# Kernel tuning notes

Hardware: AMD Instinct MI355X
Metric: run time of the kernel (lower is better)

The kernel has to match this reference:

```python
import jax, jax.numpy as jnp
import numpy as np
from jax import lax

B, C, H, L = 4, 64, 8, 2048  # batch, per-head channels, heads, sequence length


def setup_inputs() -> dict:
    key = jax.random.key(0)
    ks = jax.random.split(key, 15)

    def p(k, shape, s=0.05):
        return jax.random.normal(k, shape, jnp.float32) * s

    inp = {"x": jax.random.normal(ks[0], (B, C, L), jnp.float32)}
    for i, nm in enumerate(["q", "k", "v"]):
        inp[f"{nm}_dw"] = p(ks[1 + 4 * i], (C, 1, 3))       # depthwise conv weight, groups=C, k=3
        inp[f"{nm}_db"] = p(ks[2 + 4 * i], (C,))
        inp[f"{nm}_pw"] = p(ks[3 + 4 * i], (H * C, C))      # pointwise 1x1 conv weight
        inp[f"{nm}_pb"] = p(ks[4 + 4 * i], (H * C,))
    inp["u_w"] = p(ks[13], (C, H * C))                      # unify_heads 1x1 conv weight
    inp["u_b"] = p(ks[14], (C,))
    return inp


def dsconv(x, dw, db, pw, pb):
    # Depth-separable conv1d: depthwise (k=3, pad=1, groups=C) then pointwise 1x1.
    c = x.shape[1]
    y = lax.conv_general_dilated(x, dw, window_strides=(1,), padding=[(1, 1)],
                                 dimension_numbers=("NCH", "OIH", "NCH"),
                                 feature_group_count=c)
    y = y + db[None, :, None]
    return jnp.einsum("bcl,oc->bol", y, pw) + pb[None, :, None]


def reference(x, q_dw, q_db, q_pw, q_pb, k_dw, k_db, k_pw, k_pb,
              v_dw, v_db, v_pw, v_pb, u_w, u_b):
    b, c, l = x.shape
    h = H
    scale = c ** (-0.25)
    q = dsconv(x, q_dw, q_db, q_pw, q_pb).reshape(b, h, c, l) * scale
    k = dsconv(x, k_dw, k_db, k_pw, k_pb).reshape(b, h, c, l) * scale
    v = dsconv(x, v_dw, v_db, v_pw, v_pb).reshape(b, h, c, l)
    # dot[b,h,i,j] = sum_c k[b,h,c,i] * q[b,h,c,j]  (i = key pos, j = query pos)
    dot = jnp.einsum("bhci,bhcj->bhij", k, q)
    att = jax.nn.softmax(dot, axis=2)  # normalize over key positions (torch dim=1 of [bh,l,l])
    out = jnp.einsum("bhci,bhij->bhcj", v, att).reshape(b, h * c, l)
    return jnp.einsum("bkl,ck->bcl", out, u_w) + u_b[None, :, None]
```

## Files before the change

### kernel.cpp

```cpp
#include <hip/hip_runtime.h>
#include <hip/hip_bf16.h>
#include <stdint.h>
#include <string.h>

typedef unsigned short u16;
typedef unsigned int u32;
typedef __bf16 bf16x8 __attribute__((ext_vector_type(8)));
typedef float f32x4 __attribute__((ext_vector_type(4)));
typedef unsigned int u32x2v __attribute__((ext_vector_type(2)));

#define NB 4
#define NC 64
#define NH 8
#define NL 2048
#define HC 512

#define XT_OFF  ((size_t)0)
#define WM_OFF  ((size_t)1 << 20)
#define PBM_OFF ((size_t)2 << 20)
#define V_OFF   ((size_t)4 << 20)
#define QT_OFF  ((size_t)12 << 20)
#define KT_OFF  ((size_t)20 << 20)

#define LP 68

#if __has_builtin(__builtin_amdgcn_exp2f)
#define EXP2F __builtin_amdgcn_exp2f
#else
#define EXP2F exp2f
#endif

static __device__ __forceinline__ u16 f2bfu(float f) {
  union { float f; unsigned int i; } x; x.f = f;
  unsigned int i = x.i;
  return (u16)((i + 0x7fffu + ((i >> 16) & 1u)) >> 16);
}
static __device__ __forceinline__ u32 pk2(float a, float b) {
  float2 f; f.x = a; f.y = b;
  __hip_bfloat162 h = __float22bfloat162_rn(f);
  u32 w; __builtin_memcpy(&w, &h, 4); return w;
}
static __device__ __forceinline__ bf16x8 ld_bf8(const u16* p) {
  bf16x8 v; __builtin_memcpy(&v, p, 16); return v;
}
static __device__ __forceinline__ bf16x8 frag_from4(u32 a, u32 b, u32 c, u32 d) {
  u32 t[4] = {a, b, c, d};
  bf16x8 v; __builtin_memcpy(&v, t, 16); return v;
}

#define XCHG(X_, Y_, Fa_, Fb_)                                              \
  {                                                                         \
    u32x2v a_ = __builtin_amdgcn_permlane32_swap((X_), (Y_), false, false); \
    u32x2v b_ = __builtin_amdgcn_permlane16_swap(a_.x, a_.y, false, false); \
    Fa_ = b_.x; Fb_ = b_.y;                                                 \
  }

__global__ __launch_bounds__(256) void prep_all(
    const float* __restrict__ x,
    const float* __restrict__ qdw, const float* __restrict__ qdb,
    const float* __restrict__ qpw, const float* __restrict__ qpb,
    const float* __restrict__ kdw, const float* __restrict__ kdb,
    const float* __restrict__ kpw, const float* __restrict__ kpb,
    const float* __restrict__ vdw, const float* __restrict__ vdb,
    const float* __restrict__ vpw, const float* __restrict__ vpb,
    const float* __restrict__ ub,
    u16* __restrict__ Wm, float* __restrict__ pbm,
    u16* __restrict__ xT, float* __restrict__ out)
{
  __shared__ __align__(16) u16 T[64 * LP];
  int bx = blockIdx.x;
  int tid = threadIdx.x;

  if (bx < 512) {
    int i4 = bx * 256 + tid;
    int c = (i4 >> 9) & 63;
    float f = ub[c];
    float4 v = {f, f, f, f};
    ((float4*)out)[i4] = v;
    return;
  }
  if (bx < 902) {
    int idx = (bx - 512) * 256 + tid;
    if (idx < 98304) {
      int tns = idx >> 15, r = idx & 32767, o = r >> 6, c = r & 63;
      const float* dw = (tns == 0) ? qdw : (tns == 1) ? kdw : vdw;
      const float* pw = (tns == 0) ? qpw : (tns == 1) ? kpw : vpw;
      float s = (tns == 0) ? 0.35355339059327373f * 1.4426950408889634f
              : (tns == 1) ? 0.35355339059327373f : 1.0f;
      float w = pw[o * 64 + c] * s;
#pragma unroll
      for (int d = 0; d < 3; ++d)
        Wm[((size_t)(tns * 3 + d) * 512 + o) * 64 + c] = f2bfu(w * dw[c * 3 + d]);
    } else {
      int i = idx - 98304;
      int tns = i >> 9, o = i & 511;
      const float* db = (tns == 0) ? qdb : (tns == 1) ? kdb : vdb;
      const float* pw = (tns == 0) ? qpw : (tns == 1) ? kpw : vpw;
      const float* pb = (tns == 0) ? qpb : (tns == 1) ? kpb : vpb;
      float s = (tns == 0) ? 0.35355339059327373f * 1.4426950408889634f
              : (tns == 1) ? 0.35355339059327373f : 1.0f;
      float bias = pb[o];
      for (int c = 0; c < 64; ++c) bias += pw[o * 64 + c] * db[c];
      pbm[i] = bias * s;
    }
    return;
  }
  {
    int b2 = bx - 902;
    int lt = b2 & 31, b = b2 >> 5;
    {
      int c = tid & 63, ls = (tid >> 6) * 16;
      const float4* g = (const float4*)(x + ((size_t)b * NC + c) * NL + lt * 64 + ls);
      u16 tmp[16];
#pragma unroll
      for (int j4 = 0; j4 < 4; ++j4) {
        float4 f = g[j4];
        tmp[j4*4+0] = f2bfu(f.x); tmp[j4*4+1] = f2bfu(f.y);
        tmp[j4*4+2] = f2bfu(f.z); tmp[j4*4+3] = f2bfu(f.w);
      }
#pragma unroll
      for (int j = 0; j < 16; ++j) T[(ls + j) * LP + c] = tmp[j];
    }
    __syncthreads();
    {
      int r = tid >> 2, cs = (tid & 3) * 16;
      uint4 a = *(const uint4*)&T[r * LP + cs];
      uint4 b3 = *(const uint4*)&T[r * LP + cs + 8];
      u16* o = xT + ((size_t)b * NL + lt * 64 + r) * 64 + cs;
      *(uint4*)o = a;
      *(uint4*)(o + 8) = b3;
    }
  }
}

__global__ __launch_bounds__(256) void qkv_gemm(
    const u16* __restrict__ xT, const u16* __restrict__ Wm,
    const float* __restrict__ pbm,
    u16* __restrict__ v, u16* __restrict__ qT, u16* __restrict__ kT)
{
  __shared__ __align__(16) u16 WS[3][64 * LP];
  __shared__ __align__(16) u16 XS[2][66 * LP];
  __shared__ __align__(16) u16 OS[64 * LP];

  int bx = blockIdx.x;
  int lg  = bx & 7;
  int och = (bx >> 3) & 7;
  int tmp = bx >> 6;
  int tns = tmp % 3;
  int b   = tmp / 3;

  int tid = threadIdx.x;
  int wave = tid >> 6, lane = tid & 63, quad = lane >> 4, l16 = lane & 15;
  const u16* xg = xT + (size_t)b * NL * 64;

  {
    const u16* wg = Wm + ((size_t)(tns * 3) * 512 + och * 64) * 64;
#pragma unroll
    for (int it = 0; it < 6; ++it) {
      int s = tid + it * 256;
      int d = s >> 9, r = s & 511;
      int o = r >> 3, c4 = r & 7;
      uint4 w = *(const uint4*)(wg + ((size_t)d * 512 + o) * 64 + c4 * 8);
      *(uint4*)&WS[d][o * LP + c4 * 8] = w;
    }
  }

  int xr0 = tid >> 3,          xc0 = (tid & 7) * 8;
  int xr1 = (tid + 256) >> 3,  xc1 = xc0;
  int xr2 = (tid + 512) >> 3,  xc2 = xc0;
  uint4 R0, R1, R2;
  uint4 Z = {0, 0, 0, 0};

#define LOAD_XS(tt)                                                         \
  {                                                                         \
    int base = (lg * 4 + (tt)) * 64 - 1;                                    \
    int g0 = base + xr0, g1 = base + xr1, g2 = base + xr2;                  \
    R0 = ((unsigned)g0 < NL) ? *(const uint4*)(xg + (size_t)g0 * 64 + xc0) : Z; \
    R1 = ((unsigned)g1 < NL) ? *(const uint4*)(xg + (size_t)g1 * 64 + xc1) : Z; \
    if (tid < 16)                                                           \
      R2 = ((unsigned)g2 < NL) ? *(const uint4*)(xg + (size_t)g2 * 64 + xc2) : Z; \
  }
#define STORE_XS(bf)                                                        \
  {                                                                         \
    *(uint4*)&XS[bf][xr0 * LP + xc0] = R0;                                  \
    *(uint4*)&XS[bf][xr1 * LP + xc1] = R1;                                  \
    if (tid < 16) *(uint4*)&XS[bf][xr2 * LP + xc2] = R2;                    \
  }

  LOAD_XS(0); STORE_XS(0);
  LOAD_XS(1);
  __syncthreads();

  float bias4[4];
  bf16x8 aw[3][2];
  if (tns == 2) {
    const float* pbt = pbm + tns * 512 + och * 64 + wave * 16;
#pragma unroll
    for (int rr = 0; rr < 4; ++rr) bias4[rr] = pbt[quad * 4 + rr];
#pragma unroll
    for (int d = 0; d < 3; ++d)
#pragma unroll
      for (int kh = 0; kh < 2; ++kh)
        aw[d][kh] = ld_bf8(&WS[d][(wave * 16 + l16) * LP + kh * 32 + quad * 8]);
  } else {
    const float* pbt = pbm + tns * 512 + och * 64;
#pragma unroll
    for (int nt = 0; nt < 4; ++nt) bias4[nt] = pbt[nt * 16 + l16];
  }

  for (int t = 0; t < 4; ++t) {
    int cur = t & 1;
    f32x4 acc[4] = {{0,0,0,0},{0,0,0,0},{0,0,0,0},{0,0,0,0}};

    if (tns == 2) {
#pragma unroll
      for (int nt = 0; nt < 4; ++nt)
#pragma unroll
        for (int d = 0; d < 3; ++d)
#pragma unroll
          for (int kh = 0; kh < 2; ++kh) {
            bf16x8 bx8 = ld_bf8(&XS[cur][(nt * 16 + l16 + d) * LP + kh * 32 + quad * 8]);
            acc[nt] = __builtin_amdgcn_mfma_f32_16x16x32_bf16(aw[d][kh], bx8, acc[nt], 0, 0, 0);
          }
    } else {
      bf16x8 ax[3][2];
#pragma unroll
      for (int d = 0; d < 3; ++d)
#pragma unroll
        for (int kh = 0; kh < 2; ++kh)
          ax[d][kh] = ld_bf8(&XS[cur][(wave * 16 + l16 + d) * LP + kh * 32 + quad * 8]);
#pragma unroll
      for (int nt = 0; nt < 4; ++nt)
#pragma unroll
        for (int d = 0; d < 3; ++d)
#pragma unroll
          for (int kh = 0; kh < 2; ++kh) {
            bf16x8 bw = ld_bf8(&WS[d][(nt * 16 + l16) * LP + kh * 32 + quad * 8]);
            acc[nt] = __builtin_amdgcn_mfma_f32_16x16x32_bf16(ax[d][kh], bw, acc[nt], 0, 0, 0);
          }
    }

    if (t < 3) { STORE_XS((t + 1) & 1); if (t < 2) LOAD_XS(t + 2); }
    __syncthreads();

    if (tns == 2) {
#pragma unroll
      for (int nt = 0; nt < 4; ++nt)
#pragma unroll
        for (int rr = 0; rr < 4; ++rr)
          OS[(wave * 16 + quad * 4 + rr) * LP + nt * 16 + l16] =
              f2bfu(acc[nt][rr] + bias4[rr]);
    } else {
#pragma unroll
      for (int nt = 0; nt < 4; ++nt)
#pragma unroll
        for (int rr = 0; rr < 4; ++rr)
          OS[(wave * 16 + quad * 4 + rr) * LP + nt * 16 + l16] =
              f2bfu(acc[nt][rr] + bias4[nt]);
    }
    __syncthreads();

    {
      int lt = lg * 4 + t;
      int r = tid >> 2, ck = (tid & 3) * 16;
      uint4 a = *(const uint4*)&OS[r * LP + ck];
      uint4 b2 = *(const uint4*)&OS[r * LP + ck + 8];
      u16* gp;
      if (tns == 2)
        gp = v + ((size_t)(b * HC + och * 64 + r)) * NL + lt * 64 + ck;
      else {
        u16* dst = (tns == 0) ? qT : kT;
        gp = dst + ((size_t)(b * 8 + och) * NL + lt * 64 + r) * 64 + ck;
      }
      *(uint4*)gp = a;
      *(uint4*)(gp + 8) = b2;
    }
  }
#undef LOAD_XS
#undef STORE_XS
}

__global__ __launch_bounds__(256) void attn_kernel(
    const u16* __restrict__ qT, const u16* __restrict__ kT,
    const u16* __restrict__ vg, const float* __restrict__ uw,
    float* __restrict__ outg)
{
  __shared__ __align__(16) u16 Kt[2][64 * LP];
  __shared__ __align__(16) u16 Vt[2][64 * LP];
  __shared__ __align__(16) u16 UW[64 * LP];

  int bx = blockIdx.x;
  int qt = bx & 15, bh = bx >> 4;
  int b = bh >> 3, h = bh & 7;
  int tid = threadIdx.x;
  int wave = tid >> 6, lane = tid & 63, quad = lane >> 4, l16 = lane & 15;

  const u16* Qh = qT + (size_t)bh * NL * 64;
  const u16* Kh = kT + (size_t)bh * NL * 64;
  const u16* Vh = vg + ((size_t)(b * HC + h * NC)) * NL;
  int q0 = qt * 128;

  int sr = tid >> 2, ss = (tid & 3) * 16;
  int vc = tid & 63, vk = (tid >> 6) * 16;

  {
    int c = tid >> 2, g = (tid & 3) * 16;
    const float4* s = (const float4*)(uw + (size_t)c * HC + h * 64 + g);
#pragma unroll
    for (int j = 0; j < 4; ++j) {
      float4 w = s[j];
      u16* d = &UW[c * LP + g + j * 4];
      d[0] = f2bfu(w.x); d[1] = f2bfu(w.y); d[2] = f2bfu(w.z); d[3] = f2bfu(w.w);
    }
  }

  uint4 ka, kb, va, vb;
  {
    const u16* ks = Kh + (size_t)sr * 64 + ss;
    ka = *(const uint4*)ks; kb = *(const uint4*)(ks + 8);
    const u16* vs = Vh + (size_t)vc * NL + vk;
    va = *(const uint4*)vs; vb = *(const uint4*)(vs + 8);
    *(uint4*)&Kt[0][sr * LP + ss] = ka;
    *(uint4*)&Kt[0][sr * LP + ss + 8] = kb;
    *(uint4*)&Vt[0][vc * LP + vk] = va;
    *(uint4*)&Vt[0][vc * LP + vk + 8] = vb;
    const u16* ks1 = Kh + (size_t)(64 + sr) * 64 + ss;
    ka = *(const uint4*)ks1; kb = *(const uint4*)(ks1 + 8);
    const u16* vs1 = Vh + (size_t)vc * NL + 64 + vk;
    va = *(const uint4*)vs1; vb = *(const uint4*)(vs1 + 8);
  }

  bf16x8 bq[2][2];
#pragma unroll
  for (int t = 0; t < 2; ++t)
#pragma unroll
    for (int kh = 0; kh < 2; ++kh)
      bq[t][kh] = ld_bf8(Qh + (size_t)(q0 + wave * 32 + t * 16 + l16) * 64 +
                         kh * 32 + quad * 8);

  __syncthreads();

  f32x4 o[2][4];
#pragma unroll
  for (int t = 0; t < 2; ++t)
#pragma unroll
    for (int ct = 0; ct < 4; ++ct) o[t][ct] = (f32x4){0, 0, 0, 0};
  float l_part[2] = {0.f, 0.f};

  for (int i = 0; i < 32; ++i) {
    int cur = i & 1;
    bf16x8 ak[4][2], av[4][2];
#pragma unroll
    for (int j = 0; j < 4; ++j)
#pragma unroll
      for (int kh = 0; kh < 2; ++kh) {
        ak[j][kh] = ld_bf8(&Kt[cur][(j * 16 + l16) * LP + kh * 32 + quad * 8]);
        av[j][kh] = ld_bf8(&Vt[cur][(j * 16 + l16) * LP + kh * 32 + quad * 8]);
      }

#pragma unroll
    for (int t = 0; t < 2; ++t) {
      f32x4 s[4];
      __builtin_amdgcn_s_setprio(1);
#pragma unroll
      for (int ktl = 0; ktl < 4; ++ktl) {
        f32x4 z = {0, 0, 0, 0};
        z = __builtin_amdgcn_mfma_f32_16x16x32_bf16(ak[ktl][0], bq[t][0], z, 0, 0, 0);
        z = __builtin_amdgcn_mfma_f32_16x16x32_bf16(ak[ktl][1], bq[t][1], z, 0, 0, 0);
        s[ktl] = z;
      }
      __builtin_amdgcn_s_setprio(0);
      u32 w01[4], w23[4];
#pragma unroll
      for (int ktl = 0; ktl < 4; ++ktl) {
        float p0 = EXP2F(s[ktl][0]);
        float p1 = EXP2F(s[ktl][1]);
        float p2 = EXP2F(s[ktl][2]);
        float p3 = EXP2F(s[ktl][3]);
        l_part[t] += (p0 + p1) + (p2 + p3);
        w01[ktl] = pk2(p0, p1);
        w23[ktl] = pk2(p2, p3);
      }
#pragma unroll
      for (int kh = 0; kh < 2; ++kh) {
        u32 F0, F1, F2, F3;
        XCHG(w01[2 * kh], w01[2 * kh + 1], F0, F2);
        XCHG(w23[2 * kh], w23[2 * kh + 1], F1, F3);
        bf16x8 bp = frag_from4(F0, F1, F2, F3);
        __builtin_amdgcn_s_setprio(1);
#pragma unroll
        for (int ct = 0; ct < 4; ++ct)
          o[t][ct] = __builtin_amdgcn_mfma_f32_16x16x32_bf16(av[ct][kh], bp, o[t][ct], 0, 0, 0);
        __builtin_amdgcn_s_setprio(0);
      }
    }

    if (i < 31) {
      int nxt = cur ^ 1;
      *(uint4*)&Kt[nxt][sr * LP + ss] = ka;
      *(uint4*)&Kt[nxt][sr * LP + ss + 8] = kb;
      *(uint4*)&Vt[nxt][vc * LP + vk] = va;
      *(uint4*)&Vt[nxt][vc * LP + vk + 8] = vb;
      if (i < 30) {
        int kt2 = (i + 2) * 64;
        const u16* ks = Kh + (size_t)(kt2 + sr) * 64 + ss;
        ka = *(const uint4*)ks; kb = *(const uint4*)(ks + 8);
        const u16* vs = Vh + (size_t)vc * NL + kt2 + vk;
        va = *(const uint4*)vs; vb = *(const uint4*)(vs + 8);
      }
    }
    __syncthreads();
  }

  float* ob = outg + ((size_t)b * NC) * NL;
#pragma unroll
  for (int t = 0; t < 2; ++t) {
    float lp = l_part[t];
    lp += __shfl_xor(lp, 16);
    lp += __shfl_xor(lp, 32);
    float rinv = 1.0f / lp;

    u32 w01[4], w23[4];
#pragma unroll
    for (int ct = 0; ct < 4; ++ct) {
      w01[ct] = pk2(o[t][ct][0] * rinv, o[t][ct][1] * rinv);
      w23[ct] = pk2(o[t][ct][2] * rinv, o[t][ct][3] * rinv);
    }
    bf16x8 ot[2];
#pragma unroll
    for (int kh = 0; kh < 2; ++kh) {
      u32 F0, F1, F2, F3;
      XCHG(w01[2 * kh], w01[2 * kh + 1], F0, F2);
      XCHG(w23[2 * kh], w23[2 * kh + 1], F1, F3);
      ot[kh] = frag_from4(F0, F1, F2, F3);
    }

    int qcol = q0 + wave * 32 + t * 16 + l16;
#pragma unroll
    for (int mt = 0; mt < 4; ++mt) {
      f32x4 acc = {0, 0, 0, 0};
#pragma unroll
      for (int kh = 0; kh < 2; ++kh) {
        bf16x8 a = ld_bf8(&UW[(mt * 16 + l16) * LP + kh * 32 + quad * 8]);
        acc = __builtin_amdgcn_mfma_f32_16x16x32_bf16(a, ot[kh], acc, 0, 0, 0);
      }
#pragma unroll
      for (int rr = 0; rr < 4; ++rr) {
        int c = mt * 16 + quad * 4 + rr;
        atomicAdd(&ob[(size_t)c * NL + qcol], acc[rr]);
      }
    }
  }
}

extern "C" void kernel_launch(void* const* d_in, const int* in_sizes, int n_in,
                              void* d_out, int out_size, void* d_ws, size_t ws_size,
                              hipStream_t stream) {
  (void)in_sizes; (void)n_in; (void)out_size; (void)ws_size;
  const float* x   = (const float*)d_in[0];
  const float* qdw = (const float*)d_in[1];
  const float* qdb = (const float*)d_in[2];
  const float* qpw = (const float*)d_in[3];
  const float* qpb = (const float*)d_in[4];
  const float* kdw = (const float*)d_in[5];
  const float* kdb = (const float*)d_in[6];
  const float* kpw = (const float*)d_in[7];
  const float* kpb = (const float*)d_in[8];
  const float* vdw = (const float*)d_in[9];
  const float* vdb = (const float*)d_in[10];
  const float* vpw = (const float*)d_in[11];
  const float* vpb = (const float*)d_in[12];
  const float* uw  = (const float*)d_in[13];
  const float* ub  = (const float*)d_in[14];

  char* ws = (char*)d_ws;
  u16*   xT  = (u16*)(ws + XT_OFF);
  u16*   Wm  = (u16*)(ws + WM_OFF);
  float* pbm = (float*)(ws + PBM_OFF);
  u16*   v   = (u16*)(ws + V_OFF);
  u16*   qT  = (u16*)(ws + QT_OFF);
  u16*   kT  = (u16*)(ws + KT_OFF);
  float* out = (float*)d_out;

  prep_all<<<1030, 256, 0, stream>>>(
      x, qdw, qdb, qpw, qpb, kdw, kdb, kpw, kpb, vdw, vdb, vpw, vpb,
      ub, Wm, pbm, xT, out);
  qkv_gemm<<<768, 256, 0, stream>>>(xT, Wm, pbm, v, qT, kT);
  attn_kernel<<<512, 256, 0, stream>>>(qT, kT, v, uw, out);
}
```

Measured before the change: 167.2 us.

## Use 8 waves per attention block, one 16-query tile per wave

The attention kernel now runs 512 threads (8 waves) per block instead of 256, and each wave handles a single 16-column query tile instead of two. K/V tile loads are redistributed so each thread moves one 16-byte chunk instead of two, and the s_setprio hints are removed. The aim is to cut per-wave register pressure and raise the number of resident waves to hide LDS and exp latency. The cost is that each LDS K/V fragment load is now shared by fewer MFMAs, so LDS read traffic per FLOP roughly doubles, and barriers now synchronize more waves.

```diff
diff --git a/kernel.cpp b/kernel.cpp
--- a/kernel.cpp
+++ b/kernel.cpp
@@ -280,7 +280,7 @@
 #undef STORE_XS
 }
 
-__global__ __launch_bounds__(256) void attn_kernel(
+__global__ __launch_bounds__(512, 4) void attn_kernel(
     const u16* __restrict__ qT, const u16* __restrict__ kT,
     const u16* __restrict__ vg, const float* __restrict__ uw,
     float* __restrict__ outg)
@@ -300,52 +300,39 @@
   const u16* Vh = vg + ((size_t)(b * HC + h * NC)) * NL;
   int q0 = qt * 128;
 
-  int sr = tid >> 2, ss = (tid & 3) * 16;
-  int vc = tid & 63, vk = (tid >> 6) * 16;
+  int sr = tid >> 3, ss = (tid & 7) * 8;
+  int vc = tid >> 3, vk = (tid & 7) * 8;
 
   {
-    int c = tid >> 2, g = (tid & 3) * 16;
+    int c = tid >> 3, g = (tid & 7) * 8;
     const float4* s = (const float4*)(uw + (size_t)c * HC + h * 64 + g);
-#pragma unroll
-    for (int j = 0; j < 4; ++j) {
-      float4 w = s[j];
-      u16* d = &UW[c * LP + g + j * 4];
-      d[0] = f2bfu(w.x); d[1] = f2bfu(w.y); d[2] = f2bfu(w.z); d[3] = f2bfu(w.w);
-    }
-  }
-
-  uint4 ka, kb, va, vb;
+    float4 w0 = s[0], w1 = s[1];
+    u16* d = &UW[c * LP + g];
+    d[0] = f2bfu(w0.x); d[1] = f2bfu(w0.y); d[2] = f2bfu(w0.z); d[3] = f2bfu(w0.w);
+    d[4] = f2bfu(w1.x); d[5] = f2bfu(w1.y); d[6] = f2bfu(w1.z); d[7] = f2bfu(w1.w);
+  }
+
+  uint4 ka, va;
   {
-    const u16* ks = Kh + (size_t)sr * 64 + ss;
-    ka = *(const uint4*)ks; kb = *(const uint4*)(ks + 8);
-    const u16* vs = Vh + (size_t)vc * NL + vk;
-    va = *(const uint4*)vs; vb = *(const uint4*)(vs + 8);
+    ka = *(const uint4*)(Kh + (size_t)sr * 64 + ss);
+    va = *(const uint4*)(Vh + (size_t)vc * NL + vk);
     *(uint4*)&Kt[0][sr * LP + ss] = ka;
-    *(uint4*)&Kt[0][sr * LP + ss + 8] = kb;
     *(uint4*)&Vt[0][vc * LP + vk] = va;
-    *(uint4*)&Vt[0][vc * LP + vk + 8] = vb;
-    const u16* ks1 = Kh + (size_t)(64 + sr) * 64 + ss;
-    ka = *(const uint4*)ks1; kb = *(const uint4*)(ks1 + 8);
-    const u16* vs1 = Vh + (size_t)vc * NL + 64 + vk;
-    va = *(const uint4*)vs1; vb = *(const uint4*)(vs1 + 8);
-  }
-
-  bf16x8 bq[2][2];
-#pragma unroll
-  for (int t = 0; t < 2; ++t)
-#pragma unroll
-    for (int kh = 0; kh < 2; ++kh)
-      bq[t][kh] = ld_bf8(Qh + (size_t)(q0 + wave * 32 + t * 16 + l16) * 64 +
-                         kh * 32 + quad * 8);
+    ka = *(const uint4*)(Kh + (size_t)(64 + sr) * 64 + ss);
+    va = *(const uint4*)(Vh + (size_t)vc * NL + 64 + vk);
+  }
+
+  bf16x8 bq[2];
+#pragma unroll
+  for (int kh = 0; kh < 2; ++kh)
+    bq[kh] = ld_bf8(Qh + (size_t)(q0 + wave * 16 + l16) * 64 + kh * 32 + quad * 8);
 
   __syncthreads();
 
-  f32x4 o[2][4];
-#pragma unroll
-  for (int t = 0; t < 2; ++t)
-#pragma unroll
-    for (int ct = 0; ct < 4; ++ct) o[t][ct] = (f32x4){0, 0, 0, 0};
-  float l_part[2] = {0.f, 0.f};
+  f32x4 o[4];
+#pragma unroll
+  for (int ct = 0; ct < 4; ++ct) o[ct] = (f32x4){0, 0, 0, 0};
+  float l_part = 0.f;
 
   for (int i = 0; i < 32; ++i) {
     int cur = i & 1;
@@ -358,64 +345,52 @@
         av[j][kh] = ld_bf8(&Vt[cur][(j * 16 + l16) * LP + kh * 32 + quad * 8]);
       }
 
-#pragma unroll
-    for (int t = 0; t < 2; ++t) {
-      f32x4 s[4];
-      __builtin_amdgcn_s_setprio(1);
-#pragma unroll
-      for (int ktl = 0; ktl < 4; ++ktl) {
-        f32x4 z = {0, 0, 0, 0};
-        z = __builtin_amdgcn_mfma_f32_16x16x32_bf16(ak[ktl][0], bq[t][0], z, 0, 0, 0);
-        z = __builtin_amdgcn_mfma_f32_16x16x32_bf16(ak[ktl][1], bq[t][1], z, 0, 0, 0);
-        s[ktl] = z;
-      }
-      __builtin_amdgcn_s_setprio(0);
-      u32 w01[4], w23[4];
-#pragma unroll
-      for (int ktl = 0; ktl < 4; ++ktl) {
-        float p0 = EXP2F(s[ktl][0]);
-        float p1 = EXP2F(s[ktl][1]);
-        float p2 = EXP2F(s[ktl][2]);
-        float p3 = EXP2F(s[ktl][3]);
-        l_part[t] += (p0 + p1) + (p2 + p3);
-        w01[ktl] = pk2(p0, p1);
-        w23[ktl] = pk2(p2, p3);
-      }
-#pragma unroll
-      for (int kh = 0; kh < 2; ++kh) {
-        u32 F0, F1, F2, F3;
-        XCHG(w01[2 * kh], w01[2 * kh + 1], F0, F2);
-        XCHG(w23[2 * kh], w23[2 * kh + 1], F1, F3);
-        bf16x8 bp = frag_from4(F0, F1, F2, F3);
-        __builtin_amdgcn_s_setprio(1);
-#pragma unroll
-        for (int ct = 0; ct < 4; ++ct)
-          o[t][ct] = __builtin_amdgcn_mfma_f32_16x16x32_bf16(av[ct][kh], bp, o[t][ct], 0, 0, 0);
-        __builtin_amdgcn_s_setprio(0);
-      }
+    f32x4 s[4];
+#pragma unroll
+    for (int ktl = 0; ktl < 4; ++ktl) {
+      f32x4 z = {0, 0, 0, 0};
+      z = __builtin_amdgcn_mfma_f32_16x16x32_bf16(ak[ktl][0], bq[0], z, 0, 0, 0);
+      z = __builtin_amdgcn_mfma_f32_16x16x32_bf16(ak[ktl][1], bq[1], z, 0, 0, 0);
+      s[ktl] = z;
+    }
+    u32 w01[4], w23[4];
+#pragma unroll
+    for (int ktl = 0; ktl < 4; ++ktl) {
+      float p0 = EXP2F(s[ktl][0]);
+      float p1 = EXP2F(s[ktl][1]);
+      float p2 = EXP2F(s[ktl][2]);
+      float p3 = EXP2F(s[ktl][3]);
+      l_part += (p0 + p1) + (p2 + p3);
+      w01[ktl] = pk2(p0, p1);
+      w23[ktl] = pk2(p2, p3);
+    }
+#pragma unroll
+    for (int kh = 0; kh < 2; ++kh) {
+      u32 F0, F1, F2, F3;
+      XCHG(w01[2 * kh], w01[2 * kh + 1], F0, F2);
+      XCHG(w23[2 * kh], w23[2 * kh + 1], F1, F3);
+      bf16x8 bp = frag_from4(F0, F1, F2, F3);
+#pragma unroll
+      for (int ct = 0; ct < 4; ++ct)
+        o[ct] = __builtin_amdgcn_mfma_f32_16x16x32_bf16(av[ct][kh], bp, o[ct], 0, 0, 0);
     }
 
     if (i < 31) {
       int nxt = cur ^ 1;
       *(uint4*)&Kt[nxt][sr * LP + ss] = ka;
-      *(uint4*)&Kt[nxt][sr * LP + ss + 8] = kb;
       *(uint4*)&Vt[nxt][vc * LP + vk] = va;
-      *(uint4*)&Vt[nxt][vc * LP + vk + 8] = vb;
       if (i < 30) {
         int kt2 = (i + 2) * 64;
-        const u16* ks = Kh + (size_t)(kt2 + sr) * 64 + ss;
-        ka = *(const uint4*)ks; kb = *(const uint4*)(ks + 8);
-        const u16* vs = Vh + (size_t)vc * NL + kt2 + vk;
-        va = *(const uint4*)vs; vb = *(const uint4*)(vs + 8);
+        ka = *(const uint4*)(Kh + (size_t)(kt2 + sr) * 64 + ss);
+        va = *(const uint4*)(Vh + (size_t)vc * NL + kt2 + vk);
       }
     }
     __syncthreads();
   }
 
   float* ob = outg + ((size_t)b * NC) * NL;
-#pragma unroll
-  for (int t = 0; t < 2; ++t) {
-    float lp = l_part[t];
+  {
+    float lp = l_part;
     lp += __shfl_xor(lp, 16);
     lp += __shfl_xor(lp, 32);
     float rinv = 1.0f / lp;
@@ -423,8 +398,8 @@
     u32 w01[4], w23[4];
 #pragma unroll
     for (int ct = 0; ct < 4; ++ct) {
-      w01[ct] = pk2(o[t][ct][0] * rinv, o[t][ct][1] * rinv);
-      w23[ct] = pk2(o[t][ct][2] * rinv, o[t][ct][3] * rinv);
+      w01[ct] = pk2(o[ct][0] * rinv, o[ct][1] * rinv);
+      w23[ct] = pk2(o[ct][2] * rinv, o[ct][3] * rinv);
     }
     bf16x8 ot[2];
 #pragma unroll
@@ -435,7 +410,7 @@
       ot[kh] = frag_from4(F0, F1, F2, F3);
     }
 
-    int qcol = q0 + wave * 32 + t * 16 + l16;
+    int qcol = q0 + wave * 16 + l16;
 #pragma unroll
     for (int mt = 0; mt < 4; ++mt) {
       f32x4 acc = {0, 0, 0, 0};
@@ -486,5 +461,5 @@
       x, qdw, qdb, qpw, qpb, kdw, kdb, kpw, kpb, vdw, vdb, vpw, vpb,
       ub, Wm, pbm, xT, out);
   qkv_gemm<<<768, 256, 0, stream>>>(xT, Wm, pbm, v, qT, kT);
-  attn_kernel<<<512, 256, 0, stream>>>(qT, kT, v, uw, out);
-}
+  attn_kernel<<<512, 512, 0, stream>>>(qT, kT, v, uw, out);
+}
```

Result: faster. 153.7 us (-8.1%).
